# Optimization experiments

Measured on AMD Instinct MI355X. Metric: run time of the kernel, lower is better.

Reference implementation:

```python
import jax, jax.numpy as jnp
import numpy as np

TOKEN_DIM = 512
ATTN_DIM = 512
NUM_HEADS = 8
MLP_SIZE = 2048
EPS = 1e-6


def setup_inputs() -> dict:
    key = jax.random.key(0)
    ks = jax.random.split(key, 9)
    s_tok = 1.0 / np.sqrt(TOKEN_DIM)
    s_att = 1.0 / np.sqrt(ATTN_DIM)
    s_mlp = 1.0 / np.sqrt(MLP_SIZE)
    return {
        "inputs": jax.random.normal(ks[0], (2, 4096, TOKEN_DIM), dtype=jnp.float32),
        "Wq": jax.random.uniform(ks[1], (TOKEN_DIM, ATTN_DIM), jnp.float32, -s_tok, s_tok),
        "Wk": jax.random.uniform(ks[2], (TOKEN_DIM, ATTN_DIM), jnp.float32, -s_tok, s_tok),
        "Wv": jax.random.uniform(ks[3], (TOKEN_DIM, ATTN_DIM), jnp.float32, -s_tok, s_tok),
        "Wo": jax.random.uniform(ks[4], (ATTN_DIM, TOKEN_DIM), jnp.float32, -s_att, s_att),
        "W1": jax.random.uniform(ks[5], (TOKEN_DIM, MLP_SIZE), jnp.float32, -s_tok, s_tok),
        "b1": jax.random.uniform(ks[6], (MLP_SIZE,), jnp.float32, -s_tok, s_tok),
        "W2": jax.random.uniform(ks[7], (MLP_SIZE, TOKEN_DIM), jnp.float32, -s_mlp, s_mlp),
        "b2": jax.random.uniform(ks[8], (TOKEN_DIM,), jnp.float32, -s_mlp, s_mlp),
        "ln_att_g": jnp.ones((TOKEN_DIM,), jnp.float32),
        "ln_att_b": jnp.zeros((TOKEN_DIM,), jnp.float32),
        "ln_mlp_g": jnp.ones((TOKEN_DIM,), jnp.float32),
        "ln_mlp_b": jnp.zeros((TOKEN_DIM,), jnp.float32),
    }


def _layernorm(x, g, b):
    mu = jnp.mean(x, axis=-1, keepdims=True)
    var = jnp.mean(jnp.square(x - mu), axis=-1, keepdims=True)
    return (x - mu) * jax.lax.rsqrt(var + EPS) * g + b


def _attention(x, Wq, Wk, Wv, Wo):
    B, N, _ = x.shape
    H, Dh = NUM_HEADS, ATTN_DIM // NUM_HEADS
    # project then split heads: (B, N, H, Dh) -> (B, H, N, Dh)
    q = (x @ Wq).reshape(B, N, H, Dh).transpose(0, 2, 1, 3)
    k = (x @ Wk).reshape(B, N, H, Dh).transpose(0, 2, 1, 3)
    v = (x @ Wv).reshape(B, N, H, Dh).transpose(0, 2, 1, 3)
    scale = Dh ** -0.5
    scores = jnp.einsum("bhnd,bhmd->bhnm", q, k) * scale  # full NxN scores
    attn = jax.nn.softmax(scores, axis=-1)
    out = jnp.einsum("bhnm,bhmd->bhnd", attn, v)
    out = out.transpose(0, 2, 1, 3).reshape(B, N, ATTN_DIM)
    return out @ Wo


def reference(inputs, Wq, Wk, Wv, Wo, W1, b1, W2, b2,
              ln_att_g, ln_att_b, ln_mlp_g, ln_mlp_b):
    x = _layernorm(inputs, ln_att_g, ln_att_b)
    x = _attention(x, Wq, Wk, Wv, Wo)
    y = x + inputs
    z = _layernorm(y, ln_mlp_g, ln_mlp_b)
    z = jax.nn.gelu(z @ W1 + b1, approximate=False) @ W2 + b2
    return z + y
```

## Files before the change

### kernel.cpp

```cpp
#include <hip/hip_runtime.h>
#include <hip/hip_bf16.h>
#include <cmath>


typedef unsigned short u16;
typedef float  f32x4  __attribute__((ext_vector_type(4)));
typedef short  bf16x8 __attribute__((ext_vector_type(8)));
typedef u16    u16x4  __attribute__((ext_vector_type(4)));

#define DEV __device__ __forceinline__
#define AS1(p) ((const __attribute__((address_space(1))) void*)(p))
#define AS3(p) ((__attribute__((address_space(3))) void*)(p))

static constexpr int Mrows = 8192;
static constexpr int Dtok  = 512;
static constexpr int Fmlp  = 2048;
static constexpr float LOG2E = 1.44269504088896340736f;

DEV u16 f2b(float f) {
  union { float f; unsigned u; } v; v.f = f;
  unsigned r = v.u + 0x7fffu + ((v.u >> 16) & 1u);
  return (u16)(r >> 16);
}

DEV float b2f(u16 x) {
  union { unsigned u; float f; } v; v.u = ((unsigned)x) << 16; return v.f;
}

DEV unsigned cvtpk(float a, float b) {
  unsigned r;
  asm("v_cvt_pk_bf16_f32 %0, %1, %2" : "=v"(r) : "v"(a), "v"(b));
  return r;
}

DEV void plswap16(unsigned &a, unsigned &b) {
  asm("v_permlane16_swap_b32 %0, %1" : "+v"(a), "+v"(b));
}

DEV float ex2(float x) {
#if __has_builtin(__builtin_amdgcn_exp2f)
  return __builtin_amdgcn_exp2f(x);
#else
  float r; asm("v_exp_f32 %0, %1" : "=v"(r) : "v"(x)); return r;
#endif
}

DEV float rcp(float x) {
  float r; asm("v_rcp_f32 %0, %1" : "=v"(r) : "v"(x)); return r;
}

DEV float gelu(float x) {
  const float u = x * x;
  float z = x * (2.30225828f + 0.10295048f * u);
  z = fminf(z, 80.0f);
  const float E = ex2(z);
  return x * E * rcp(E + 1.0f);
}

DEV f32x4 mfma32(bf16x8 a, bf16x8 b, f32x4 c) {
  return __builtin_amdgcn_mfma_f32_16x16x32_bf16(a, b, c, 0, 0, 0);
}

__global__ __launch_bounds__(256) void convert_ln(
    const float* __restrict__ Wq, const float* __restrict__ Wk,
    const float* __restrict__ Wv, const float* __restrict__ Wo,
    const float* __restrict__ W1, const float* __restrict__ W2,
    u16* __restrict__ Wqt, u16* __restrict__ Wkt, u16* __restrict__ Wvt,
    u16* __restrict__ Wot, u16* __restrict__ W1t, u16* __restrict__ W2t,
    float qscale,
    const float* __restrict__ xin, const float* __restrict__ g1,
    const float* __restrict__ be1, u16* __restrict__ xln) {
  int bid = blockIdx.x;
  const int tid = threadIdx.x;
  if (bid >= 12288) {
    const int row = bid - 12288;
    float2 v = ((const float2*)(xin + (size_t)row * 512))[tid];
    float s = v.x + v.y, ss = v.x * v.x + v.y * v.y;
#pragma unroll
    for (int off = 32; off > 0; off >>= 1) {
      s  += __shfl_down(s, off);
      ss += __shfl_down(ss, off);
    }
    __shared__ float ps[4], pss[4];
    const int wave = tid >> 6, lane = tid & 63;
    if (lane == 0) { ps[wave] = s; pss[wave] = ss; }
    __syncthreads();
    const float S  = ps[0] + ps[1] + ps[2] + ps[3];
    const float SS = pss[0] + pss[1] + pss[2] + pss[3];
    const float mean = S * (1.0f / 512.0f);
    const float var  = SS * (1.0f / 512.0f) - mean * mean;
    const float rstd = rsqrtf(var + 1e-6f);
    const float2 gg = ((const float2*)g1)[tid];
    const float2 bb = ((const float2*)be1)[tid];
    ushort2 ov;
    ov.x = f2b((v.x - mean) * rstd * gg.x + bb.x);
    ov.y = f2b((v.y - mean) * rstd * gg.y + bb.y);
    ((ushort2*)(xln + (size_t)row * 512))[tid] = ov;
    return;
  }
  const float* src; u16* dst; int K, N; float sc = 1.0f;
  if (bid < 1024)      { src = Wq; dst = Wqt; K = 512;  N = 512;  sc = qscale; }
  else if (bid < 2048) { src = Wk; dst = Wkt; K = 512;  N = 512;  bid -= 1024; }
  else if (bid < 3072) { src = Wv; dst = Wvt; K = 512;  N = 512;  bid -= 2048; }
  else if (bid < 4096) { src = Wo; dst = Wot; K = 512;  N = 512;  bid -= 3072; }
  else if (bid < 8192) { src = W1; dst = W1t; K = 512;  N = 2048; bid -= 4096; }
  else                 { src = W2; dst = W2t; K = 2048; N = 512;  bid -= 8192; }
  const int idx = bid * 256 + tid;
  const int k = idx / N, n = idx - k * N;
  dst[(size_t)n * K + k] = f2b(src[idx] * sc);
}

__global__ __launch_bounds__(256) void ln_bf16(const u16* __restrict__ x,
                                               const float* __restrict__ g,
                                               const float* __restrict__ b,
                                               u16* __restrict__ o) {
  const int row = blockIdx.x, tid = threadIdx.x;
  const ushort2 v2 = ((const ushort2*)(x + (size_t)row * 512))[tid];
  const float vx = b2f(v2.x), vy = b2f(v2.y);
  float s = vx + vy, ss = vx * vx + vy * vy;
#pragma unroll
  for (int off = 32; off > 0; off >>= 1) {
    s  += __shfl_down(s, off);
    ss += __shfl_down(ss, off);
  }
  __shared__ float ps[4], pss[4];
  const int wave = tid >> 6, lane = tid & 63;
  if (lane == 0) { ps[wave] = s; pss[wave] = ss; }
  __syncthreads();
  const float S  = ps[0] + ps[1] + ps[2] + ps[3];
  const float SS = pss[0] + pss[1] + pss[2] + pss[3];
  const float mean = S * (1.0f / 512.0f);
  const float var  = SS * (1.0f / 512.0f) - mean * mean;
  const float rstd = rsqrtf(var + 1e-6f);
  const float2 gg = ((const float2*)g)[tid];
  const float2 bb = ((const float2*)b)[tid];
  ushort2 ov;
  ov.x = f2b((vx - mean) * rstd * gg.x + bb.x);
  ov.y = f2b((vy - mean) * rstd * gg.y + bb.y);
  ((ushort2*)(o + (size_t)row * 512))[tid] = ov;
}

template <int EPI, int BM>
__global__ __launch_bounds__(256) void gemm_kernel(
    const u16* __restrict__ A, const u16* __restrict__ Bt,
    u16* __restrict__ outb, u16* __restrict__ outbK, u16* __restrict__ outbV,
    float* __restrict__ outf,
    const float* __restrict__ bias,
    const float* __restrict__ residf, const u16* __restrict__ residb,
    int M, int N, int K) {
  __shared__ u16 Al[2][BM * 32];
  __shared__ u16 Bl[2][128 * 32];
  constexpr int WM = BM / 2;
  const int tid = threadIdx.x;
  const int wave = tid >> 6, lane = tid & 63;
  const int lhi = lane >> 4, llo = lane & 15;
  const int wr = wave >> 1, wc = wave & 1;
  const int m0 = blockIdx.y * BM, n0 = blockIdx.x * 128;

  f32x4 acc[BM / 32][4] = {};

  auto stageG = [&](int k0, int Bf) {
#pragma unroll
    for (int i = 0; i < BM / 64; ++i) {
      const int rb = i * 64 + wave * 16;
      const u16* sa = A + (size_t)(m0 + rb + (lane >> 2)) * K + k0 + (lane & 3) * 8;
      __builtin_amdgcn_global_load_lds(AS1(sa), AS3(&Al[Bf][rb * 32]), 16, 0, 0);
    }
#pragma unroll
    for (int i = 0; i < 2; ++i) {
      const int rb = i * 64 + wave * 16;
      const u16* sb = Bt + (size_t)(n0 + rb + (lane >> 2)) * K + k0 + (lane & 3) * 8;
      __builtin_amdgcn_global_load_lds(AS1(sb), AS3(&Bl[Bf][rb * 32]), 16, 0, 0);
    }
  };

  auto computeG = [&](int Bf) {
    bf16x8 af[BM / 32], bfr[4];
#pragma unroll
    for (int mi = 0; mi < BM / 32; ++mi)
      af[mi] = *(const bf16x8*)&Al[Bf][(wr * WM + mi * 16 + llo) * 32 + lhi * 8];
#pragma unroll
    for (int ni = 0; ni < 4; ++ni)
      bfr[ni] = *(const bf16x8*)&Bl[Bf][(wc * 64 + ni * 16 + llo) * 32 + lhi * 8];
#pragma unroll
    for (int mi = 0; mi < BM / 32; ++mi)
#pragma unroll
      for (int ni = 0; ni < 4; ++ni)
        acc[mi][ni] = __builtin_amdgcn_mfma_f32_16x16x32_bf16(af[mi], bfr[ni],
                                                              acc[mi][ni], 0, 0, 0);
  };

  stageG(0, 0);
  __syncthreads();
  for (int k0 = 0; k0 < K; k0 += 64) {
    stageG(k0 + 32, 1);
    computeG(0);
    __syncthreads();
    if (k0 + 64 < K) stageG(k0 + 64, 0);
    computeG(1);
    __syncthreads();
  }

  if constexpr (EPI == 5) {
    if (n0 < 1024) {
      u16* dst = (n0 < 512) ? outb : outbK;
      const int c0 = (n0 & 511) + wc * 64;
#pragma unroll
      for (int mi = 0; mi < BM / 32; ++mi)
#pragma unroll
        for (int r = 0; r < 4; ++r) {
          const size_t grow = (size_t)m0 + wr * WM + mi * 16 + lhi * 4 + r;
#pragma unroll
          for (int ni = 0; ni < 4; ++ni)
            dst[grow * 512 + c0 + ni * 16 + llo] = f2b(acc[mi][ni][r]);
        }
    } else {
      const int bb = m0 >> 12;
      const int nb = (m0 & 4095) + wr * WM + lhi * 4;
#pragma unroll
      for (int mi = 0; mi < BM / 32; ++mi)
#pragma unroll
        for (int ni = 0; ni < 4; ++ni) {
          const int gcol = (n0 - 1024) + wc * 64 + ni * 16 + llo;
          u16x4 pk;
#pragma unroll
          for (int r = 0; r < 4; ++r) pk[r] = f2b(acc[mi][ni][r]);
          u16* dst = outbV + (((size_t)(bb * 8 + (gcol >> 6))) * 64 + (gcol & 63)) * 4096
                           + nb + mi * 16;
          *(u16x4*)dst = pk;
        }
    }
  } else {
#pragma unroll
    for (int mi = 0; mi < BM / 32; ++mi) {
#pragma unroll
      for (int r = 0; r < 4; ++r) {
        const size_t grow = (size_t)m0 + wr * WM + mi * 16 + lhi * 4 + r;
#pragma unroll
        for (int ni = 0; ni < 4; ++ni) {
          const int gcol = n0 + wc * 64 + ni * 16 + llo;
          float v = acc[mi][ni][r];
          if (EPI == 1) {
            v = gelu(v + bias[gcol]);
            outb[grow * N + gcol] = f2b(v);
          } else if (EPI == 2) {
            v += residf[grow * N + gcol];
            outb[grow * N + gcol] = f2b(v);
          } else {
            v += bias[gcol] + b2f(residb[grow * N + gcol]);
            outf[grow * N + gcol] = v;
          }
        }
      }
    }
  }
}

__global__ __launch_bounds__(256) void attn_kernel(const u16* __restrict__ Q,
                                                   const u16* __restrict__ Kg,
                                                   const u16* __restrict__ VT,
                                                   u16* __restrict__ O) {
  const int qt = blockIdx.x, bh = blockIdx.y;
  const int b = bh >> 3, h = bh & 7;
  const int tid = threadIdx.x, wave = tid >> 6, lane = tid & 63;
  const int lhi = lane >> 4, llo = lane & 15;

  __shared__ u16 Kl[2][4096];
  __shared__ u16 Vl[2][4096];

  const size_t rowbase = (size_t)b * 4096;
  const int col0 = h * 64;
  const int q0 = qt * 128;

  bf16x8 qf0[2], qf1[2];
  {
    const u16* qp0 = Q + (rowbase + q0 + wave * 32 + llo) * 512 + col0 + lhi * 8;
    qf0[0] = *(const bf16x8*)qp0;
    qf0[1] = *(const bf16x8*)(qp0 + 32);
    const u16* qp1 = qp0 + (size_t)16 * 512;
    qf1[0] = *(const bf16x8*)qp1;
    qf1[1] = *(const bf16x8*)(qp1 + 32);
  }

  const int srow8 = lane >> 3;
  const int kcsw  = ((lane & 7) ^ srow8) * 8;
  const u16* kbase0 = Kg + (rowbase + wave * 16 + srow8) * 512 + col0 + kcsw;
  const u16* kbase1 = kbase0 + (size_t)8 * 512;
  const u16* vbase0 = VT + ((size_t)bh * 64 + wave * 16 + srow8) * 4096 + kcsw;
  const u16* vbase1 = vbase0 + (size_t)8 * 4096;

  const int xr = (llo & 7) << 4;
  const int ka0 = (16 * lhi) ^ xr;
  const int ka1 = (16 * (4 + lhi)) ^ xr;
  const int csig = ((lhi & 1) << 1) | (lhi >> 1);
  const int vb0 = 16 * (csig ^ (llo & 7));
  const int vb1 = 16 * ((csig | 4) ^ (llo & 7));

  const bf16x8 ones = {(short)0x3F80, (short)0x3F80, (short)0x3F80, (short)0x3F80,
                       (short)0x3F80, (short)0x3F80, (short)0x3F80, (short)0x3F80};

  f32x4 o0[4] = {}, o1[4] = {};
  f32x4 o40 = {}, o41 = {};

  auto stage = [&](int kvr, int B) {
    __builtin_amdgcn_global_load_lds(AS1(kbase0 + (size_t)kvr * 512),
                                     AS3(&Kl[B][wave * 1024]), 16, 0, 0);
    __builtin_amdgcn_global_load_lds(AS1(kbase1 + (size_t)kvr * 512),
                                     AS3(&Kl[B][wave * 1024 + 512]), 16, 0, 0);
    __builtin_amdgcn_global_load_lds(AS1(vbase0 + kvr),
                                     AS3(&Vl[B][wave * 1024]), 16, 0, 0);
    __builtin_amdgcn_global_load_lds(AS1(vbase1 + kvr),
                                     AS3(&Vl[B][wave * 1024 + 512]), 16, 0, 0);
  };

  auto packP = [&](const f32x4* stj, bf16x8& Bv0, bf16x8& Bv1) {
    unsigned a0 = cvtpk(ex2(stj[0][0]), ex2(stj[0][1]));
    unsigned a1 = cvtpk(ex2(stj[0][2]), ex2(stj[0][3]));
    unsigned b0 = cvtpk(ex2(stj[1][0]), ex2(stj[1][1]));
    unsigned b1 = cvtpk(ex2(stj[1][2]), ex2(stj[1][3]));
    unsigned c0 = cvtpk(ex2(stj[2][0]), ex2(stj[2][1]));
    unsigned c1 = cvtpk(ex2(stj[2][2]), ex2(stj[2][3]));
    unsigned d0 = cvtpk(ex2(stj[3][0]), ex2(stj[3][1]));
    unsigned d1 = cvtpk(ex2(stj[3][2]), ex2(stj[3][3]));
    plswap16(a0, b0); plswap16(a1, b1);
    plswap16(c0, d0); plswap16(c1, d1);
    union UB { unsigned u[4]; bf16x8 v; } X, Y;
    X.u[0] = a0; X.u[1] = a1; X.u[2] = b0; X.u[3] = b1;
    Y.u[0] = c0; Y.u[1] = c1; Y.u[2] = d0; Y.u[3] = d1;
    Bv0 = X.v; Bv1 = Y.v;
  };

  auto compute = [&](int B) {
    const char* klb = (const char*)&Kl[B][0] + llo * 128;
    const char* vlb = (const char*)&Vl[B][0] + llo * 128;
    f32x4 st0[4], st1[4];
    __builtin_amdgcn_s_setprio(1);
#pragma unroll
    for (int jt = 0; jt < 4; ++jt) {
      bf16x8 kf0 = *(const bf16x8*)(klb + jt * 2048 + ka0);
      bf16x8 kf1 = *(const bf16x8*)(klb + jt * 2048 + ka1);
      f32x4 z0 = {}, z1 = {};
      z0 = mfma32(kf0, qf0[0], z0); z0 = mfma32(kf1, qf0[1], z0);
      z1 = mfma32(kf0, qf1[0], z1); z1 = mfma32(kf1, qf1[1], z1);
      st0[jt] = z0; st1[jt] = z1;
    }
    __builtin_amdgcn_s_setprio(0);
    bf16x8 P00, P01, P10, P11;
    packP(st0, P00, P01);
    packP(st1, P10, P11);
    __builtin_amdgcn_s_setprio(1);
    o40 = mfma32(ones, P00, o40); o40 = mfma32(ones, P01, o40);
    o41 = mfma32(ones, P10, o41); o41 = mfma32(ones, P11, o41);
#pragma unroll
    for (int dt = 0; dt < 4; ++dt) {
      bf16x8 vf0 = *(const bf16x8*)(vlb + dt * 2048 + vb0);
      bf16x8 vf1 = *(const bf16x8*)(vlb + dt * 2048 + vb1);
      o0[dt] = mfma32(vf0, P00, o0[dt]); o0[dt] = mfma32(vf1, P01, o0[dt]);
      o1[dt] = mfma32(vf0, P10, o1[dt]); o1[dt] = mfma32(vf1, P11, o1[dt]);
    }
    __builtin_amdgcn_s_setprio(0);
  };

  stage(0, 0);
  __syncthreads();
  for (int kv0 = 0; kv0 < 4096; kv0 += 128) {
    stage(kv0 + 64, 1);
    compute(0);
    __syncthreads();
    if (kv0 + 128 < 4096) stage(kv0 + 128, 0);
    compute(1);
    __syncthreads();
  }

  {
    const float inv = 1.0f / o40[0];
    u16* op = O + (rowbase + q0 + wave * 32 + llo) * 512 + col0 + 4 * lhi;
#pragma unroll
    for (int dt = 0; dt < 4; ++dt) {
      u16x4 pk;
#pragma unroll
      for (int r = 0; r < 4; ++r) pk[r] = f2b(o0[dt][r] * inv);
      *(u16x4*)(op + dt * 16) = pk;
    }
  }
  {
    const float inv = 1.0f / o41[0];
    u16* op = O + (rowbase + q0 + wave * 32 + 16 + llo) * 512 + col0 + 4 * lhi;
#pragma unroll
    for (int dt = 0; dt < 4; ++dt) {
      u16x4 pk;
#pragma unroll
      for (int r = 0; r < 4; ++r) pk[r] = f2b(o1[dt][r] * inv);
      *(u16x4*)(op + dt * 16) = pk;
    }
  }
}

extern "C" void kernel_launch(void* const* d_in, const int* in_sizes, int n_in,
                              void* d_out, int out_size, void* d_ws, size_t ws_size,
                              hipStream_t stream) {
  const float* inputs = (const float*)d_in[0];
  const float* Wq  = (const float*)d_in[1];
  const float* Wk  = (const float*)d_in[2];
  const float* Wv  = (const float*)d_in[3];
  const float* Wo  = (const float*)d_in[4];
  const float* W1  = (const float*)d_in[5];
  const float* b1  = (const float*)d_in[6];
  const float* W2  = (const float*)d_in[7];
  const float* b2  = (const float*)d_in[8];
  const float* g1  = (const float*)d_in[9];
  const float* be1 = (const float*)d_in[10];
  const float* g2  = (const float*)d_in[11];
  const float* be2 = (const float*)d_in[12];
  float* out = (float*)d_out;

  const int M = Mrows, D = Dtok, F = Fmlp;

  char* w = (char*)d_ws;
  u16* xln  = (u16*)w;  w += (size_t)M * D * 2;
  u16* Qb   = (u16*)w;  w += (size_t)M * D * 2;
  u16* Kb   = (u16*)w;  w += (size_t)M * D * 2;
  u16* VT   = (u16*)w;  w += (size_t)M * D * 2;
  u16* attn = (u16*)w;  w += (size_t)M * D * 2;
  u16* yb   = (u16*)w;  w += (size_t)M * D * 2;
  u16* Wqt  = (u16*)w;  w += (size_t)D * D * 2;
  u16* Wkt  = (u16*)w;  w += (size_t)D * D * 2;
  u16* Wvt  = (u16*)w;  w += (size_t)D * D * 2;
  u16* Wot  = (u16*)w;  w += (size_t)D * D * 2;
  u16* W1t  = (u16*)w;  w += (size_t)D * F * 2;
  u16* W2t  = (u16*)w;  w += (size_t)F * D * 2;
  u16* zln = xln;
  u16* h1  = Qb;

  convert_ln<<<dim3(12288 + 8192), 256, 0, stream>>>(
      Wq, Wk, Wv, Wo, W1, W2, Wqt, Wkt, Wvt, Wot, W1t, W2t,
      0.125f * LOG2E, inputs, g1, be1, xln);

  gemm_kernel<5, 128><<<dim3(12, M / 128), 256, 0, stream>>>(
      xln, Wqt, Qb, Kb, VT, nullptr, nullptr, nullptr, nullptr, M, 512, D);

  attn_kernel<<<dim3(32, 16), 256, 0, stream>>>(Qb, Kb, VT, attn);

  gemm_kernel<2, 64><<<dim3(4, M / 64), 256, 0, stream>>>(
      attn, Wot, yb, nullptr, nullptr, nullptr, nullptr, inputs, nullptr, M, D, D);

  ln_bf16<<<dim3(M), 256, 0, stream>>>(yb, g2, be2, zln);

  gemm_kernel<1, 128><<<dim3(16, M / 128), 256, 0, stream>>>(
      zln, W1t, h1, nullptr, nullptr, nullptr, b1, nullptr, nullptr, M, F, D);
  gemm_kernel<3, 64><<<dim3(4, M / 64), 256, 0, stream>>>(
      h1, W2t, nullptr, nullptr, nullptr, out, b2, nullptr, yb, M, D, F);
}
```

Baseline: 227.9 us.

## Double attention KV tile to 128 and transpose weights via LDS tiles

The attention kernel now stages 128 keys/values per buffer instead of 64. This halves the number of barriers and loop iterations and issues more MFMAs between syncs, with the V-slot swizzle and LDS layout reworked to match. The weight conversion kernel now transposes 64x64 tiles through shared memory, so global reads and writes are coalesced instead of scattered per element. In exchange it doubles the attention LDS footprint (64KB), which may reduce occupancy, and raises register pressure from larger score arrays.

Result: slower. 236.7 us (+3.9%).

```diff
diff --git a/kernel.cpp b/kernel.cpp
--- a/kernel.cpp
+++ b/kernel.cpp
@@ -70,10 +70,10 @@
     float qscale,
     const float* __restrict__ xin, const float* __restrict__ g1,
     const float* __restrict__ be1, u16* __restrict__ xln) {
-  int bid = blockIdx.x;
+  const int bid = blockIdx.x;
   const int tid = threadIdx.x;
-  if (bid >= 12288) {
-    const int row = bid - 12288;
+  if (bid >= 768) {
+    const int row = bid - 768;
     float2 v = ((const float2*)(xin + (size_t)row * 512))[tid];
     float s = v.x + v.y, ss = v.x * v.x + v.y * v.y;
 #pragma unroll
@@ -98,16 +98,30 @@
     ((ushort2*)(xln + (size_t)row * 512))[tid] = ov;
     return;
   }
-  const float* src; u16* dst; int K, N; float sc = 1.0f;
-  if (bid < 1024)      { src = Wq; dst = Wqt; K = 512;  N = 512;  sc = qscale; }
-  else if (bid < 2048) { src = Wk; dst = Wkt; K = 512;  N = 512;  bid -= 1024; }
-  else if (bid < 3072) { src = Wv; dst = Wvt; K = 512;  N = 512;  bid -= 2048; }
-  else if (bid < 4096) { src = Wo; dst = Wot; K = 512;  N = 512;  bid -= 3072; }
-  else if (bid < 8192) { src = W1; dst = W1t; K = 512;  N = 2048; bid -= 4096; }
-  else                 { src = W2; dst = W2t; K = 2048; N = 512;  bid -= 8192; }
-  const int idx = bid * 256 + tid;
-  const int k = idx / N, n = idx - k * N;
-  dst[(size_t)n * K + k] = f2b(src[idx] * sc);
+  __shared__ float tl[64][65];
+  const float* src; u16* dst; int K, N; float sc = 1.0f; int tk, tn;
+  if (bid < 256) {
+    const int m = bid >> 6;
+    src = (m == 0) ? Wq : (m == 1) ? Wk : (m == 2) ? Wv : Wo;
+    dst = (m == 0) ? Wqt : (m == 1) ? Wkt : (m == 2) ? Wvt : Wot;
+    K = 512; N = 512; if (m == 0) sc = qscale;
+    const int lt = bid & 63; tk = lt >> 3; tn = lt & 7;
+  } else if (bid < 512) {
+    src = W1; dst = W1t; K = 512; N = 2048;
+    const int lt = bid - 256; tk = lt >> 5; tn = lt & 31;
+  } else {
+    src = W2; dst = W2t; K = 2048; N = 512;
+    const int lt = bid - 512; tk = lt >> 3; tn = lt & 7;
+  }
+  const int k0 = tk * 64, n0 = tn * 64;
+  const int rr = tid >> 6, cc = tid & 63;
+#pragma unroll
+  for (int j = 0; j < 16; ++j)
+    tl[j * 4 + rr][cc] = src[(size_t)(k0 + j * 4 + rr) * N + n0 + cc];
+  __syncthreads();
+#pragma unroll
+  for (int j = 0; j < 16; ++j)
+    dst[(size_t)(n0 + j * 4 + rr) * K + k0 + cc] = f2b(tl[cc][j * 4 + rr] * sc);
 }
 
 __global__ __launch_bounds__(256) void ln_bf16(const u16* __restrict__ x,
@@ -265,8 +279,8 @@
   const int tid = threadIdx.x, wave = tid >> 6, lane = tid & 63;
   const int lhi = lane >> 4, llo = lane & 15;
 
-  __shared__ u16 Kl[2][4096];
-  __shared__ u16 Vl[2][4096];
+  __shared__ u16 Kl[2][8192];
+  __shared__ u16 Vl[2][8192];
 
   const size_t rowbase = (size_t)b * 4096;
   const int col0 = h * 64;
@@ -282,19 +296,30 @@
     qf1[1] = *(const bf16x8*)(qp1 + 32);
   }
 
-  const int srow8 = lane >> 3;
-  const int kcsw  = ((lane & 7) ^ srow8) * 8;
-  const u16* kbase0 = Kg + (rowbase + wave * 16 + srow8) * 512 + col0 + kcsw;
-  const u16* kbase1 = kbase0 + (size_t)8 * 512;
-  const u16* vbase0 = VT + ((size_t)bh * 64 + wave * 16 + srow8) * 4096 + kcsw;
-  const u16* vbase1 = vbase0 + (size_t)8 * 4096;
+  const u16* kb[4];
+  {
+    const int srow = lane >> 3;
+    const int csw  = ((lane & 7) ^ srow) * 8;
+#pragma unroll
+    for (int i = 0; i < 4; ++i)
+      kb[i] = Kg + (rowbase + wave * 32 + i * 8 + srow) * 512 + col0 + csw;
+  }
+  const u16* vb[4];
+  {
+    const int dr = lane >> 4;
+#pragma unroll
+    for (int i = 0; i < 4; ++i)
+      vb[i] = VT + ((size_t)bh * 64 + wave * 16 + 4 * i + dr) * 4096
+                 + 8 * ((lane & 15) ^ (4 * i + dr));
+  }
 
   const int xr = (llo & 7) << 4;
   const int ka0 = (16 * lhi) ^ xr;
   const int ka1 = (16 * (4 + lhi)) ^ xr;
   const int csig = ((lhi & 1) << 1) | (lhi >> 1);
-  const int vb0 = 16 * (csig ^ (llo & 7));
-  const int vb1 = 16 * ((csig | 4) ^ (llo & 7));
+  int vslot[4];
+#pragma unroll
+  for (int g = 0; g < 4; ++g) vslot[g] = ((4 * g + csig) ^ llo) * 16;
 
   const bf16x8 ones = {(short)0x3F80, (short)0x3F80, (short)0x3F80, (short)0x3F80,
                        (short)0x3F80, (short)0x3F80, (short)0x3F80, (short)0x3F80};
@@ -303,40 +328,38 @@
   f32x4 o40 = {}, o41 = {};
 
   auto stage = [&](int kvr, int B) {
-    __builtin_amdgcn_global_load_lds(AS1(kbase0 + (size_t)kvr * 512),
-                                     AS3(&Kl[B][wave * 1024]), 16, 0, 0);
-    __builtin_amdgcn_global_load_lds(AS1(kbase1 + (size_t)kvr * 512),
-                                     AS3(&Kl[B][wave * 1024 + 512]), 16, 0, 0);
-    __builtin_amdgcn_global_load_lds(AS1(vbase0 + kvr),
-                                     AS3(&Vl[B][wave * 1024]), 16, 0, 0);
-    __builtin_amdgcn_global_load_lds(AS1(vbase1 + kvr),
-                                     AS3(&Vl[B][wave * 1024 + 512]), 16, 0, 0);
+    u16* kd = &Kl[B][wave * 2048];
+    u16* vd = &Vl[B][wave * 2048];
+#pragma unroll
+    for (int i = 0; i < 4; ++i) {
+      __builtin_amdgcn_global_load_lds(AS1(kb[i] + (size_t)kvr * 512),
+                                       AS3(kd + i * 512), 16, 0, 0);
+      __builtin_amdgcn_global_load_lds(AS1(vb[i] + kvr),
+                                       AS3(vd + i * 512), 16, 0, 0);
+    }
   };
 
-  auto packP = [&](const f32x4* stj, bf16x8& Bv0, bf16x8& Bv1) {
-    unsigned a0 = cvtpk(ex2(stj[0][0]), ex2(stj[0][1]));
-    unsigned a1 = cvtpk(ex2(stj[0][2]), ex2(stj[0][3]));
-    unsigned b0 = cvtpk(ex2(stj[1][0]), ex2(stj[1][1]));
-    unsigned b1 = cvtpk(ex2(stj[1][2]), ex2(stj[1][3]));
-    unsigned c0 = cvtpk(ex2(stj[2][0]), ex2(stj[2][1]));
-    unsigned c1 = cvtpk(ex2(stj[2][2]), ex2(stj[2][3]));
-    unsigned d0 = cvtpk(ex2(stj[3][0]), ex2(stj[3][1]));
-    unsigned d1 = cvtpk(ex2(stj[3][2]), ex2(stj[3][3]));
-    plswap16(a0, b0); plswap16(a1, b1);
-    plswap16(c0, d0); plswap16(c1, d1);
-    union UB { unsigned u[4]; bf16x8 v; } X, Y;
-    X.u[0] = a0; X.u[1] = a1; X.u[2] = b0; X.u[3] = b1;
-    Y.u[0] = c0; Y.u[1] = c1; Y.u[2] = d0; Y.u[3] = d1;
-    Bv0 = X.v; Bv1 = Y.v;
+  auto packP = [&](const f32x4* st, bf16x8* P) {
+#pragma unroll
+    for (int g = 0; g < 4; ++g) {
+      unsigned a0 = cvtpk(ex2(st[2 * g][0]), ex2(st[2 * g][1]));
+      unsigned a1 = cvtpk(ex2(st[2 * g][2]), ex2(st[2 * g][3]));
+      unsigned b0 = cvtpk(ex2(st[2 * g + 1][0]), ex2(st[2 * g + 1][1]));
+      unsigned b1 = cvtpk(ex2(st[2 * g + 1][2]), ex2(st[2 * g + 1][3]));
+      plswap16(a0, b0); plswap16(a1, b1);
+      union UB { unsigned u[4]; bf16x8 v; } X;
+      X.u[0] = a0; X.u[1] = a1; X.u[2] = b0; X.u[3] = b1;
+      P[g] = X.v;
+    }
   };
 
   auto compute = [&](int B) {
     const char* klb = (const char*)&Kl[B][0] + llo * 128;
-    const char* vlb = (const char*)&Vl[B][0] + llo * 128;
-    f32x4 st0[4], st1[4];
+    const char* vlb = (const char*)&Vl[B][0] + llo * 256;
+    f32x4 st0[8], st1[8];
     __builtin_amdgcn_s_setprio(1);
 #pragma unroll
-    for (int jt = 0; jt < 4; ++jt) {
+    for (int jt = 0; jt < 8; ++jt) {
       bf16x8 kf0 = *(const bf16x8*)(klb + jt * 2048 + ka0);
       bf16x8 kf1 = *(const bf16x8*)(klb + jt * 2048 + ka1);
       f32x4 z0 = {}, z1 = {};
@@ -345,29 +368,34 @@
       st0[jt] = z0; st1[jt] = z1;
     }
     __builtin_amdgcn_s_setprio(0);
-    bf16x8 P00, P01, P10, P11;
-    packP(st0, P00, P01);
-    packP(st1, P10, P11);
+    bf16x8 P0[4], P1[4];
+    packP(st0, P0);
+    packP(st1, P1);
     __builtin_amdgcn_s_setprio(1);
-    o40 = mfma32(ones, P00, o40); o40 = mfma32(ones, P01, o40);
-    o41 = mfma32(ones, P10, o41); o41 = mfma32(ones, P11, o41);
+#pragma unroll
+    for (int g = 0; g < 4; ++g) {
+      o40 = mfma32(ones, P0[g], o40);
+      o41 = mfma32(ones, P1[g], o41);
+    }
 #pragma unroll
     for (int dt = 0; dt < 4; ++dt) {
-      bf16x8 vf0 = *(const bf16x8*)(vlb + dt * 2048 + vb0);
-      bf16x8 vf1 = *(const bf16x8*)(vlb + dt * 2048 + vb1);
-      o0[dt] = mfma32(vf0, P00, o0[dt]); o0[dt] = mfma32(vf1, P01, o0[dt]);
-      o1[dt] = mfma32(vf0, P10, o1[dt]); o1[dt] = mfma32(vf1, P11, o1[dt]);
+#pragma unroll
+      for (int g = 0; g < 4; ++g) {
+        bf16x8 vf = *(const bf16x8*)(vlb + dt * 4096 + vslot[g]);
+        o0[dt] = mfma32(vf, P0[g], o0[dt]);
+        o1[dt] = mfma32(vf, P1[g], o1[dt]);
+      }
     }
     __builtin_amdgcn_s_setprio(0);
   };
 
   stage(0, 0);
   __syncthreads();
-  for (int kv0 = 0; kv0 < 4096; kv0 += 128) {
-    stage(kv0 + 64, 1);
+  for (int kv0 = 0; kv0 < 4096; kv0 += 256) {
+    stage(kv0 + 128, 1);
     compute(0);
     __syncthreads();
-    if (kv0 + 128 < 4096) stage(kv0 + 128, 0);
+    if (kv0 + 256 < 4096) stage(kv0 + 256, 0);
     compute(1);
     __syncthreads();
   }
@@ -432,7 +460,7 @@
   u16* zln = xln;
   u16* h1  = Qb;
 
-  convert_ln<<<dim3(12288 + 8192), 256, 0, stream>>>(
+  convert_ln<<<dim3(768 + 8192), 256, 0, stream>>>(
       Wq, Wk, Wv, Wo, W1, W2, Wqt, Wkt, Wvt, Wot, W1t, W2t,
       0.125f * LOG2E, inputs, g1, be1, xln);
 
```
